# Kernel tuning notes

Hardware: AMD Instinct MI355X
Metric: run time of the kernel (lower is better)

The kernel has to match this reference:

```python
import jax, jax.numpy as jnp
import numpy as np

ALPHA = 2.0  # init alpha
B, N, E = 8, 100000, 3200000


def setup_inputs() -> dict:
    key = jax.random.key(0)
    k1, k2, k3, k4 = jax.random.split(key, 4)
    y = jax.random.normal(k1, (B, N), dtype=jnp.float32)
    t = jnp.zeros((1,), dtype=jnp.float32)  # unused by the math, kept for signature fidelity
    graph_edge_attr = jax.random.uniform(k2, (E,), dtype=jnp.float32)
    dist_w = jax.random.normal(k3, (E,), dtype=jnp.float32)  # distances.weight ([E,1] flattened)
    edge_index = jax.random.randint(k4, (2, E), 0, N, dtype=jnp.int64)
    return {"y": y, "t": t, "graph_edge_attr": graph_edge_attr, "dist_w": dist_w, "edge_index": edge_index}


def reference(y, t, graph_edge_attr, dist_w, edge_index):
    ei0 = edge_index[0]  # source node per edge [E]
    ei1 = edge_index[1]  # target node per edge [E]
    n = y.shape[1]
    # edge_attr = sigmoid(distances.weight) -> [E]
    edge_attr = jax.nn.sigmoid(dist_w)
    # deg = scatter_add(graph.edge_attr, edge_index[0], dim_size=N) -> [N]
    deg = jax.ops.segment_sum(graph_edge_attr, ei0, num_segments=n)
    deg_a = jnp.power(deg[ei0], ALPHA)  # [E], gathered per edge at source node
    # grad_m = sqrt(edge_attr) * -1 * min(y[:,ei1]/deg^a - y[:,ei0]/deg^a, 0) -> [B,E]
    diff = y[:, ei1] / deg_a - y[:, ei0] / deg_a
    grad_m = jnp.sqrt(edge_attr) * (-1.0) * jnp.minimum(diff, 0.0)
    # grad_norm = scatter_add(|grad_m|, ei0, dim=1, dim_size=N) -> [B,N]
    grad_norm = jnp.zeros_like(y).at[:, ei0].add(jnp.abs(grad_m))
    # run_pde is None -> return f (mask branch not taken)
    return 1.0 - grad_norm
```

## Files before the change

kernel.cpp:

```cpp
#include <hip/hip_runtime.h>
#include <hip/hip_fp16.h>

#define BATCH 8
#define S_LOG 9
#define SBUCKET 512
#define KC 256
#define CB 1024
#define TTILE 2048
#define EPT 8
#define SCAP 15360

static inline size_t alignup(size_t x) { return (x + 255) & ~(size_t)255; }

__device__ __forceinline__ unsigned bf16hi(unsigned u) {
    return (u + 0x7FFFu + ((u >> 16) & 1u)) >> 16;
}

__device__ __forceinline__ int aligned_chunk(int E) {
    return (((E + CB - 1) / CB) + 15) & ~15;
}


__global__ __launch_bounds__(256)
void count_transpose_kernel(const int* __restrict__ ei0, unsigned* __restrict__ counts,
                            const float* __restrict__ y, uint4* __restrict__ yT,
                            int E, int N, int Npad) {
    __shared__ unsigned cnt[KC];
    int tid = threadIdx.x;
    if (blockIdx.x >= CB) {
        int n = (blockIdx.x - CB) * 256 + tid;
        if (n < Npad) {
            uint4 o = make_uint4(0u, 0u, 0u, 0u);
            if (n < N) {
                unsigned p[8];
#pragma unroll
                for (int b = 0; b < BATCH; ++b)
                    p[b] = bf16hi(__float_as_uint(y[(size_t)b * N + n]));
                o = make_uint4(p[0] | (p[1] << 16), p[2] | (p[3] << 16),
                               p[4] | (p[5] << 16), p[6] | (p[7] << 16));
            }
            yT[n] = o;
        }
        return;
    }
    cnt[tid] = 0;
    __syncthreads();
    int chunk = aligned_chunk(E);
    int lo = blockIdx.x * chunk;
    int hi = min(lo + chunk, E);
    for (int bi = lo; bi < hi; bi += 1024) {
        int idx = bi + tid * 4;
        if (idx + 4 <= hi) {
            int4 v = *(const int4*)(ei0 + idx);
            atomicAdd(&cnt[(unsigned)v.x >> S_LOG], 1u);
            atomicAdd(&cnt[(unsigned)v.y >> S_LOG], 1u);
            atomicAdd(&cnt[(unsigned)v.z >> S_LOG], 1u);
            atomicAdd(&cnt[(unsigned)v.w >> S_LOG], 1u);
        } else {
#pragma unroll
            for (int j = 0; j < 4; ++j) {
                int i2 = idx + j;
                if (i2 < hi) atomicAdd(&cnt[(unsigned)ei0[i2] >> S_LOG], 1u);
            }
        }
    }
    __syncthreads();
    counts[(size_t)tid * CB + blockIdx.x] = cnt[tid];
}

__global__ __launch_bounds__(256)
void scanB1_kernel(const unsigned* __restrict__ counts, unsigned* __restrict__ base,
                   unsigned* __restrict__ tot) {
    __shared__ unsigned ssum[256];
    int k = blockIdx.x, tid = threadIdx.x;
    const uint4* row4 = (const uint4*)(counts + (size_t)k * CB);
    uint4 v = row4[tid];
    unsigned lsum = v.x + v.y + v.z + v.w;
    ssum[tid] = lsum;
    __syncthreads();
    for (int off = 1; off < 256; off <<= 1) {
        unsigned u = ssum[tid];
        unsigned a = (tid >= off) ? ssum[tid - off] : 0u;
        __syncthreads();
        ssum[tid] = u + a;
        __syncthreads();
    }
    unsigned ex = ssum[tid] - lsum;
    if (tid == 255) tot[k] = ssum[255];
    uint4 o;
    o.x = ex;
    o.y = ex + v.x;
    o.z = o.y + v.y;
    o.w = o.z + v.z;
    ((uint4*)(base + (size_t)k * CB))[tid] = o;
}

__global__ void scanC_kernel(const unsigned* __restrict__ tot,
                             unsigned* __restrict__ bb, int E, int K) {
    __shared__ unsigned sb[KC];
    int t = threadIdx.x;
    unsigned v = (t < K) ? tot[t] : 0u;
    sb[t] = v;
    __syncthreads();
    for (int off = 1; off < KC; off <<= 1) {
        unsigned u = sb[t];
        unsigned a = (t >= off) ? sb[t - off] : 0u;
        __syncthreads();
        sb[t] = u + a;
        __syncthreads();
    }
    bb[t] = sb[t] - v;
    if (t == KC - 1) bb[KC] = (unsigned)E;
}

__global__ __launch_bounds__(256)
void scatter_kernel(const int* __restrict__ ei0, const int* __restrict__ ei1,
                    const float* __restrict__ dw, const float* __restrict__ gea,
                    const unsigned* __restrict__ base, const unsigned* __restrict__ bb,
                    uint2* __restrict__ w0coef, int E) {
    __shared__ unsigned cursor[KC];
    __shared__ unsigned h[KC];
    __shared__ unsigned tstart[KC];
    __shared__ unsigned wsum[4];
    __shared__ uint2 srec[TTILE];
    __shared__ unsigned char skey[TTILE];
    int tid = threadIdx.x;
    cursor[tid] = base[(size_t)tid * CB + blockIdx.x] + bb[tid];
    int chunk = aligned_chunk(E);
    int lo = blockIdx.x * chunk;
    int hi = min(lo + chunk, E);
    __syncthreads();

    for (int tileLo = lo; tileLo < hi; tileLo += TTILE) {
        int tn = min(TTILE, hi - tileLo);
        h[tid] = 0;
        __syncthreads();

        int base_off = tid * EPT;
        unsigned k_r[EPT], w0_r[EPT], pk_r[EPT], rk_r[EPT];
        int s0a[EPT], s1a[EPT];
        float dwa[EPT], gea_a[EPT];
        bool anyv = base_off < tn;
        if (base_off + EPT <= tn) {
            const int4* p0 = (const int4*)(ei0 + tileLo + base_off);
            const int4* p1 = (const int4*)(ei1 + tileLo + base_off);
            const float4* pd = (const float4*)(dw + tileLo + base_off);
            const float4* pg = (const float4*)(gea + tileLo + base_off);
            int4 a0 = p0[0], a1 = p0[1];
            int4 b0 = p1[0], b1 = p1[1];
            float4 d0 = pd[0], d1 = pd[1];
            float4 g0 = pg[0], g1 = pg[1];
            s0a[0]=a0.x; s0a[1]=a0.y; s0a[2]=a0.z; s0a[3]=a0.w;
            s0a[4]=a1.x; s0a[5]=a1.y; s0a[6]=a1.z; s0a[7]=a1.w;
            s1a[0]=b0.x; s1a[1]=b0.y; s1a[2]=b0.z; s1a[3]=b0.w;
            s1a[4]=b1.x; s1a[5]=b1.y; s1a[6]=b1.z; s1a[7]=b1.w;
            dwa[0]=d0.x; dwa[1]=d0.y; dwa[2]=d0.z; dwa[3]=d0.w;
            dwa[4]=d1.x; dwa[5]=d1.y; dwa[6]=d1.z; dwa[7]=d1.w;
            gea_a[0]=g0.x; gea_a[1]=g0.y; gea_a[2]=g0.z; gea_a[3]=g0.w;
            gea_a[4]=g1.x; gea_a[5]=g1.y; gea_a[6]=g1.z; gea_a[7]=g1.w;
#pragma unroll
            for (int j = 0; j < EPT; ++j) k_r[j] = 0u;
#pragma unroll
            for (int j = 0; j < EPT; ++j) {
                unsigned k = (unsigned)s0a[j] >> S_LOG;
                unsigned s0l = (unsigned)(s0a[j] & (SBUCKET - 1));
                k_r[j] = k;
                w0_r[j] = (unsigned)s1a[j] | (s0l << 17);
                float sig = 1.0f / (1.0f + __expf(-dwa[j]));
                pk_r[j] = (bf16hi(__float_as_uint(sqrtf(sig))) << 16) |
                          bf16hi(__float_as_uint(gea_a[j]));
            }
#pragma unroll
            for (int j = 0; j < EPT; ++j)
                rk_r[j] = atomicAdd(&h[k_r[j]], 1u);
        } else {
#pragma unroll
            for (int j = 0; j < EPT; ++j) {
                int off = base_off + j;
                k_r[j] = 0xFFFFFFFFu;
                if (off < tn) {
                    int i = tileLo + off;
                    int s0v = ei0[i];
                    int s1v = ei1[i];
                    unsigned k = (unsigned)s0v >> S_LOG;
                    unsigned s0l = (unsigned)(s0v & (SBUCKET - 1));
                    k_r[j] = k;
                    w0_r[j] = (unsigned)s1v | (s0l << 17);
                    float sig = 1.0f / (1.0f + __expf(-dw[i]));
                    pk_r[j] = (bf16hi(__float_as_uint(sqrtf(sig))) << 16) |
                              bf16hi(__float_as_uint(gea[i]));
                }
            }
#pragma unroll
            for (int j = 0; j < EPT; ++j)
                if (k_r[j] != 0xFFFFFFFFu) rk_r[j] = atomicAdd(&h[k_r[j]], 1u);
        }
        bool fullv = base_off + EPT <= tn;
        __syncthreads();

        unsigned hv = h[tid];
        unsigned v = hv;
        unsigned lane = tid & 63;
        unsigned wv = tid >> 6;
#pragma unroll
        for (int off = 1; off < 64; off <<= 1) {
            unsigned t = __shfl_up(v, off, 64);
            if (lane >= off) v += t;
        }
        if (lane == 63) wsum[wv] = v;
        __syncthreads();
        unsigned addv = 0;
#pragma unroll
        for (unsigned w = 0; w < 4; ++w)
            if (w < wv) addv += wsum[w];
        tstart[tid] = v + addv - hv;
        __syncthreads();

        if (fullv) {
#pragma unroll
            for (int j = 0; j < EPT; ++j) {
                unsigned slot = tstart[k_r[j]] + rk_r[j];
                srec[slot] = make_uint2(w0_r[j], pk_r[j]);
                skey[slot] = (unsigned char)k_r[j];
            }
        } else if (anyv) {
#pragma unroll
            for (int j = 0; j < EPT; ++j)
                if (k_r[j] != 0xFFFFFFFFu) {
                    unsigned slot = tstart[k_r[j]] + rk_r[j];
                    srec[slot] = make_uint2(w0_r[j], pk_r[j]);
                    skey[slot] = (unsigned char)k_r[j];
                }
        }
        __syncthreads();

        for (int i = tid; i < tn; i += 256) {
            uint2 u = srec[i];
            unsigned k = skey[i];
            unsigned pos = cursor[k] + ((unsigned)i - tstart[k]);
            w0coef[pos] = u;
        }
        __syncthreads();
        cursor[tid] += h[tid];
        __syncthreads();
    }
}

__global__ __launch_bounds__(512)
void accum_kernel(const uint2* __restrict__ w0coef, const unsigned* __restrict__ bb,
                  const uint4* __restrict__ yT,
                  float* __restrict__ out, int N) {
    __shared__ uint2 srt[SCAP];
    __shared__ unsigned bcnt[SBUCKET];
    __shared__ unsigned boff[SBUCKET];
    __shared__ unsigned bcur[SBUCKET];
    __shared__ unsigned wsums[8];
    int k = blockIdx.x, tid = threadIdx.x;
    int n0 = k << S_LOG;
    unsigned lane = tid & 63;
    unsigned wvi = tid >> 6;

    unsigned lo = bb[k], hi = bb[k + 1];

    uint4 y0r = yT[n0 + tid];
    float y0f[8];
    {
        unsigned yw[4] = {y0r.x, y0r.y, y0r.z, y0r.w};
#pragma unroll
        for (int p = 0; p < 4; ++p) {
            y0f[2 * p]     = __uint_as_float(yw[p] << 16);
            y0f[2 * p + 1] = __uint_as_float(yw[p] & 0xFFFF0000u);
        }
    }
    float acc[8] = {0.f, 0.f, 0.f, 0.f, 0.f, 0.f, 0.f, 0.f};
    float dega = 0.f;

    for (unsigned cbase = lo; cbase < hi; cbase += SCAP) {
        unsigned cn = min((unsigned)SCAP, hi - cbase);
        bcnt[tid] = 0u;
        __syncthreads();
        for (unsigned i = tid; i < cn; i += 512)
            atomicAdd(&bcnt[w0coef[cbase + i].x >> 17], 1u);
        __syncthreads();
        unsigned myc = bcnt[tid];
        unsigned v = myc;
#pragma unroll
        for (int off = 1; off < 64; off <<= 1) {
            unsigned t = __shfl_up(v, off, 64);
            if (lane >= off) v += t;
        }
        if (lane == 63) wsums[wvi] = v;
        __syncthreads();
        unsigned add = 0;
#pragma unroll
        for (unsigned w = 0; w < 8; ++w)
            if (w < wvi) add += wsums[w];
        unsigned myoff = v + add - myc;
        boff[tid] = myoff;
        bcur[tid] = myoff;
        __syncthreads();
        for (unsigned i = tid; i < cn; i += 512) {
            uint2 r = w0coef[cbase + i];
            unsigned slot = atomicAdd(&bcur[r.x >> 17], 1u);
            srt[slot] = r;
        }
        __syncthreads();
        unsigned s = myoff, e = myoff + myc;
        uint2 r0 = make_uint2(0u, 0u), r1 = make_uint2(0u, 0u);
        uint4 g0 = make_uint4(0u, 0u, 0u, 0u), g1 = g0;
        if (s < e)     { r0 = srt[s];     g0 = yT[r0.x & 0x1FFFFu]; }
        if (s + 1 < e) { r1 = srt[s + 1]; g1 = yT[r1.x & 0x1FFFFu]; }
        for (unsigned i = s; i < e; ++i) {
            uint2 rc = r0; uint4 gc = g0;
            r0 = r1; g0 = g1;
            if (i + 2 < e) { r1 = srt[i + 2]; g1 = yT[r1.x & 0x1FFFFu]; }
            float cf = __uint_as_float(rc.y & 0xFFFF0000u);
            float ge = __uint_as_float(rc.y << 16);
            unsigned gw[4] = {gc.x, gc.y, gc.z, gc.w};
#pragma unroll
            for (int p = 0; p < 4; ++p) {
                float ga = __uint_as_float(gw[p] << 16);
                float gb = __uint_as_float(gw[p] & 0xFFFF0000u);
                acc[2 * p]     += cf * fmaxf(y0f[2 * p]     - ga, 0.0f);
                acc[2 * p + 1] += cf * fmaxf(y0f[2 * p + 1] - gb, 0.0f);
            }
            dega += ge;
        }
        __syncthreads();
    }

    int n = n0 + tid;
    if (n < N) {
        float invd = (dega != 0.0f) ? 1.0f / (dega * dega) : 0.0f;
#pragma unroll
        for (int b = 0; b < BATCH; ++b)
            out[(size_t)b * N + n] = 1.0f - acc[b] * invd;
    }
}


__global__ void fill_one_kernel(float* __restrict__ out, int n) {
    int i = blockIdx.x * blockDim.x + threadIdx.x;
    if (i < n) out[i] = 1.0f;
}

__global__ void zero_kernel(float* __restrict__ p, int n) {
    int i = blockIdx.x * blockDim.x + threadIdx.x;
    if (i < n) p[i] = 0.0f;
}

__global__ void deg_kernel(const float* __restrict__ gea,
                           const int* __restrict__ ei0,
                           float* __restrict__ deg, int E) {
    int e = blockIdx.x * blockDim.x + threadIdx.x;
    if (e < E) atomicAdd(&deg[ei0[e]], gea[e]);
}

__global__ void edge_kernel(const float* __restrict__ y,
                            const float* __restrict__ dw,
                            const int* __restrict__ ei0,
                            const int* __restrict__ ei1,
                            const float* __restrict__ deg,
                            float* __restrict__ out,
                            int E, int N) {
    int e = blockIdx.x * blockDim.x + threadIdx.x;
    if (e >= E) return;
    int s0 = ei0[e];
    int s1 = ei1[e];
    float d = deg[s0];
    float inv = 1.0f / (d * d);
    float sig = 1.0f / (1.0f + __expf(-dw[e]));
    float coef = sqrtf(sig) * inv;
#pragma unroll
    for (int b = 0; b < BATCH; ++b) {
        float y0 = y[(size_t)b * N + s0];
        float y1 = y[(size_t)b * N + s1];
        float gm = coef * fmaxf(y0 - y1, 0.0f);
        if (gm != 0.0f) atomicAdd(&out[(size_t)b * N + s0], -gm);
    }
}


extern "C" void kernel_launch(void* const* d_in, const int* in_sizes, int n_in,
                              void* d_out, int out_size, void* d_ws, size_t ws_size,
                              hipStream_t stream) {
    const float* y   = (const float*)d_in[0];
    const float* gea = (const float*)d_in[2];
    const float* dw  = (const float*)d_in[3];
    const int*   ei  = (const int*)d_in[4];

    const int E = in_sizes[2];
    const int N = in_sizes[0] / BATCH;
    const int* ei0 = ei;
    const int* ei1 = ei + E;

    const int K = (N + SBUCKET - 1) >> S_LOG;
    const int Npad = K << S_LOG;

    size_t o_yT     = 0;
    size_t o_rcf    = o_yT     + alignup((size_t)Npad * 16);
    size_t o_counts = o_rcf    + alignup((size_t)E * 8);
    size_t o_base   = o_counts + alignup((size_t)KC * CB * 4);
    size_t o_tot    = o_base   + alignup((size_t)KC * CB * 4);
    size_t o_bb     = o_tot    + alignup((size_t)KC * 4);
    size_t need     = o_bb     + alignup((size_t)(KC + 1) * 4);

    if (K <= KC && N <= 131071 && ws_size >= need) {
        char* w = (char*)d_ws;
        uint4*    yT     = (uint4*)(w + o_yT);
        uint2*    w0coef = (uint2*)(w + o_rcf);
        unsigned* counts = (unsigned*)(w + o_counts);
        unsigned* base   = (unsigned*)(w + o_base);
        unsigned* tot    = (unsigned*)(w + o_tot);
        unsigned* bb     = (unsigned*)(w + o_bb);

        int tb = (Npad + 255) / 256;
        count_transpose_kernel<<<CB + tb, 256, 0, stream>>>(ei0, counts, y, yT,
                                                            E, N, Npad);
        scanB1_kernel<<<K, 256, 0, stream>>>(counts, base, tot);
        scanC_kernel<<<1, KC, 0, stream>>>(tot, bb, E, K);
        scatter_kernel<<<CB, 256, 0, stream>>>(ei0, ei1, dw, gea, base, bb,
                                               w0coef, E);
        accum_kernel<<<K, 512, 0, stream>>>(w0coef, bb, yT, (float*)d_out, N);
    } else {
        float* deg = (float*)d_ws;
        zero_kernel<<<(N + 255) / 256, 256, 0, stream>>>(deg, N);
        fill_one_kernel<<<(out_size + 255) / 256, 256, 0, stream>>>((float*)d_out, out_size);
        deg_kernel<<<(E + 255) / 256, 256, 0, stream>>>(gea, ei0, deg, E);
        edge_kernel<<<(E + 255) / 256, 256, 0, stream>>>(y, dw, ei0, ei1, deg,
                                                         (float*)d_out, E, N);
    }
}
```

Measured before the change: 154.2 us.

## Replace bucketed two-level sort with per-node CSR counting sort via global atomics

Drops the coarse 512-node bucket histogram, the tiled shared-memory scatter and the per-block local sort in the accumulator. It now builds a full per-node CSR: global atomic degree counts, a two-level scan over nodes, and a scatter that places each edge directly with a global atomic cursor. The accumulator becomes one thread per node walking its contiguous edge range, with no shared-memory staging. This removes several shared-memory passes and barriers, but adds about 6.4M global atomics and uncoalesced 8-byte scattered writes, and each thread's edge-list length now depends on node degree, so work per thread is uneven.

After: 503.2 us. 3.26x slower.

```diff
diff --git a/kernel.cpp b/kernel.cpp
--- a/kernel.cpp
+++ b/kernel.cpp
@@ -6,9 +6,7 @@
 #define SBUCKET 512
 #define KC 256
 #define CB 1024
-#define TTILE 2048
 #define EPT 8
-#define SCAP 15360
 
 static inline size_t alignup(size_t x) { return (x + 255) & ~(size_t)255; }
 
@@ -22,10 +20,15 @@
 
 
 __global__ __launch_bounds__(256)
-void count_transpose_kernel(const int* __restrict__ ei0, unsigned* __restrict__ counts,
+void zero_deg_kernel(unsigned* __restrict__ deg, int Npad) {
+    int i = blockIdx.x * 256 + threadIdx.x;
+    if (i < Npad) deg[i] = 0u;
+}
+
+__global__ __launch_bounds__(256)
+void count_transpose_kernel(const int* __restrict__ ei0, unsigned* __restrict__ deg,
                             const float* __restrict__ y, uint4* __restrict__ yT,
                             int E, int N, int Npad) {
-    __shared__ unsigned cnt[KC];
     int tid = threadIdx.x;
     if (blockIdx.x >= CB) {
         int n = (blockIdx.x - CB) * 256 + tid;
@@ -43,8 +46,6 @@
         }
         return;
     }
-    cnt[tid] = 0;
-    __syncthreads();
     int chunk = aligned_chunk(E);
     int lo = blockIdx.x * chunk;
     int hi = min(lo + chunk, E);
@@ -52,51 +53,47 @@
         int idx = bi + tid * 4;
         if (idx + 4 <= hi) {
             int4 v = *(const int4*)(ei0 + idx);
-            atomicAdd(&cnt[(unsigned)v.x >> S_LOG], 1u);
-            atomicAdd(&cnt[(unsigned)v.y >> S_LOG], 1u);
-            atomicAdd(&cnt[(unsigned)v.z >> S_LOG], 1u);
-            atomicAdd(&cnt[(unsigned)v.w >> S_LOG], 1u);
+            atomicAdd(&deg[v.x], 1u);
+            atomicAdd(&deg[v.y], 1u);
+            atomicAdd(&deg[v.z], 1u);
+            atomicAdd(&deg[v.w], 1u);
         } else {
 #pragma unroll
             for (int j = 0; j < 4; ++j) {
                 int i2 = idx + j;
-                if (i2 < hi) atomicAdd(&cnt[(unsigned)ei0[i2] >> S_LOG], 1u);
+                if (i2 < hi) atomicAdd(&deg[ei0[i2]], 1u);
             }
         }
     }
+}
+
+__global__ __launch_bounds__(512)
+void scanN1_kernel(const unsigned* __restrict__ deg, unsigned* __restrict__ node_base,
+                   unsigned* __restrict__ tot) {
+    __shared__ unsigned wsums[8];
+    int k = blockIdx.x, tid = threadIdx.x;
+    unsigned lane = tid & 63;
+    unsigned wvi = tid >> 6;
+    int i = (k << S_LOG) + tid;
+    unsigned dv = deg[i];
+    unsigned v = dv;
+#pragma unroll
+    for (int off = 1; off < 64; off <<= 1) {
+        unsigned t = __shfl_up(v, off, 64);
+        if (lane >= off) v += t;
+    }
+    if (lane == 63) wsums[wvi] = v;
     __syncthreads();
-    counts[(size_t)tid * CB + blockIdx.x] = cnt[tid];
-}
-
-__global__ __launch_bounds__(256)
-void scanB1_kernel(const unsigned* __restrict__ counts, unsigned* __restrict__ base,
-                   unsigned* __restrict__ tot) {
-    __shared__ unsigned ssum[256];
-    int k = blockIdx.x, tid = threadIdx.x;
-    const uint4* row4 = (const uint4*)(counts + (size_t)k * CB);
-    uint4 v = row4[tid];
-    unsigned lsum = v.x + v.y + v.z + v.w;
-    ssum[tid] = lsum;
-    __syncthreads();
-    for (int off = 1; off < 256; off <<= 1) {
-        unsigned u = ssum[tid];
-        unsigned a = (tid >= off) ? ssum[tid - off] : 0u;
-        __syncthreads();
-        ssum[tid] = u + a;
-        __syncthreads();
-    }
-    unsigned ex = ssum[tid] - lsum;
-    if (tid == 255) tot[k] = ssum[255];
-    uint4 o;
-    o.x = ex;
-    o.y = ex + v.x;
-    o.z = o.y + v.y;
-    o.w = o.z + v.z;
-    ((uint4*)(base + (size_t)k * CB))[tid] = o;
+    unsigned add = 0;
+#pragma unroll
+    for (unsigned w = 0; w < 8; ++w)
+        if (w < wvi) add += wsums[w];
+    node_base[i] = v + add - dv;
+    if (tid == 511) tot[k] = v + add;
 }
 
 __global__ void scanC_kernel(const unsigned* __restrict__ tot,
-                             unsigned* __restrict__ bb, int E, int K) {
+                             unsigned* __restrict__ bb, int K) {
     __shared__ unsigned sb[KC];
     int t = threadIdx.x;
     unsigned v = (t < K) ? tot[t] : 0u;
@@ -110,46 +107,39 @@
         __syncthreads();
     }
     bb[t] = sb[t] - v;
-    if (t == KC - 1) bb[KC] = (unsigned)E;
+}
+
+__global__ __launch_bounds__(512)
+void scanN2_kernel(unsigned* __restrict__ node_base, unsigned* __restrict__ node_cur,
+                   const unsigned* __restrict__ bb) {
+    int k = blockIdx.x, tid = threadIdx.x;
+    int i = (k << S_LOG) + tid;
+    unsigned v = node_base[i] + bb[k];
+    node_base[i] = v;
+    node_cur[i] = v;
 }
 
 __global__ __launch_bounds__(256)
 void scatter_kernel(const int* __restrict__ ei0, const int* __restrict__ ei1,
                     const float* __restrict__ dw, const float* __restrict__ gea,
-                    const unsigned* __restrict__ base, const unsigned* __restrict__ bb,
-                    uint2* __restrict__ w0coef, int E) {
-    __shared__ unsigned cursor[KC];
-    __shared__ unsigned h[KC];
-    __shared__ unsigned tstart[KC];
-    __shared__ unsigned wsum[4];
-    __shared__ uint2 srec[TTILE];
-    __shared__ unsigned char skey[TTILE];
+                    unsigned* __restrict__ node_cur, uint2* __restrict__ w0coef, int E) {
     int tid = threadIdx.x;
-    cursor[tid] = base[(size_t)tid * CB + blockIdx.x] + bb[tid];
     int chunk = aligned_chunk(E);
     int lo = blockIdx.x * chunk;
     int hi = min(lo + chunk, E);
-    __syncthreads();
-
-    for (int tileLo = lo; tileLo < hi; tileLo += TTILE) {
-        int tn = min(TTILE, hi - tileLo);
-        h[tid] = 0;
-        __syncthreads();
-
-        int base_off = tid * EPT;
-        unsigned k_r[EPT], w0_r[EPT], pk_r[EPT], rk_r[EPT];
-        int s0a[EPT], s1a[EPT];
-        float dwa[EPT], gea_a[EPT];
-        bool anyv = base_off < tn;
-        if (base_off + EPT <= tn) {
-            const int4* p0 = (const int4*)(ei0 + tileLo + base_off);
-            const int4* p1 = (const int4*)(ei1 + tileLo + base_off);
-            const float4* pd = (const float4*)(dw + tileLo + base_off);
-            const float4* pg = (const float4*)(gea + tileLo + base_off);
+
+    for (int base_i = lo + tid * EPT; base_i < hi; base_i += 256 * EPT) {
+        if (base_i + EPT <= hi) {
+            const int4* p0 = (const int4*)(ei0 + base_i);
+            const int4* p1 = (const int4*)(ei1 + base_i);
+            const float4* pd = (const float4*)(dw + base_i);
+            const float4* pg = (const float4*)(gea + base_i);
             int4 a0 = p0[0], a1 = p0[1];
             int4 b0 = p1[0], b1 = p1[1];
             float4 d0 = pd[0], d1 = pd[1];
             float4 g0 = pg[0], g1 = pg[1];
+            int s0a[EPT], s1a[EPT];
+            float dwa[EPT], gea_a[EPT];
             s0a[0]=a0.x; s0a[1]=a0.y; s0a[2]=a0.z; s0a[3]=a0.w;
             s0a[4]=a1.x; s0a[5]=a1.y; s0a[6]=a1.z; s0a[7]=a1.w;
             s1a[0]=b0.x; s1a[1]=b0.y; s1a[2]=b0.z; s1a[3]=b0.w;
@@ -158,111 +148,41 @@
             dwa[4]=d1.x; dwa[5]=d1.y; dwa[6]=d1.z; dwa[7]=d1.w;
             gea_a[0]=g0.x; gea_a[1]=g0.y; gea_a[2]=g0.z; gea_a[3]=g0.w;
             gea_a[4]=g1.x; gea_a[5]=g1.y; gea_a[6]=g1.z; gea_a[7]=g1.w;
-#pragma unroll
-            for (int j = 0; j < EPT; ++j) k_r[j] = 0u;
+            unsigned pk[EPT], pos[EPT];
 #pragma unroll
             for (int j = 0; j < EPT; ++j) {
-                unsigned k = (unsigned)s0a[j] >> S_LOG;
-                unsigned s0l = (unsigned)(s0a[j] & (SBUCKET - 1));
-                k_r[j] = k;
-                w0_r[j] = (unsigned)s1a[j] | (s0l << 17);
                 float sig = 1.0f / (1.0f + __expf(-dwa[j]));
-                pk_r[j] = (bf16hi(__float_as_uint(sqrtf(sig))) << 16) |
-                          bf16hi(__float_as_uint(gea_a[j]));
+                pk[j] = (bf16hi(__float_as_uint(sqrtf(sig))) << 16) |
+                        bf16hi(__float_as_uint(gea_a[j]));
             }
 #pragma unroll
             for (int j = 0; j < EPT; ++j)
-                rk_r[j] = atomicAdd(&h[k_r[j]], 1u);
+                pos[j] = atomicAdd(&node_cur[s0a[j]], 1u);
+#pragma unroll
+            for (int j = 0; j < EPT; ++j)
+                w0coef[pos[j]] = make_uint2((unsigned)s1a[j], pk[j]);
         } else {
 #pragma unroll
             for (int j = 0; j < EPT; ++j) {
-                int off = base_off + j;
-                k_r[j] = 0xFFFFFFFFu;
-                if (off < tn) {
-                    int i = tileLo + off;
-                    int s0v = ei0[i];
-                    int s1v = ei1[i];
-                    unsigned k = (unsigned)s0v >> S_LOG;
-                    unsigned s0l = (unsigned)(s0v & (SBUCKET - 1));
-                    k_r[j] = k;
-                    w0_r[j] = (unsigned)s1v | (s0l << 17);
+                int i = base_i + j;
+                if (i < hi) {
                     float sig = 1.0f / (1.0f + __expf(-dw[i]));
-                    pk_r[j] = (bf16hi(__float_as_uint(sqrtf(sig))) << 16) |
-                              bf16hi(__float_as_uint(gea[i]));
+                    unsigned pk = (bf16hi(__float_as_uint(sqrtf(sig))) << 16) |
+                                  bf16hi(__float_as_uint(gea[i]));
+                    unsigned pos = atomicAdd(&node_cur[ei0[i]], 1u);
+                    w0coef[pos] = make_uint2((unsigned)ei1[i], pk);
                 }
             }
-#pragma unroll
-            for (int j = 0; j < EPT; ++j)
-                if (k_r[j] != 0xFFFFFFFFu) rk_r[j] = atomicAdd(&h[k_r[j]], 1u);
-        }
-        bool fullv = base_off + EPT <= tn;
-        __syncthreads();
-
-        unsigned hv = h[tid];
-        unsigned v = hv;
-        unsigned lane = tid & 63;
-        unsigned wv = tid >> 6;
-#pragma unroll
-        for (int off = 1; off < 64; off <<= 1) {
-            unsigned t = __shfl_up(v, off, 64);
-            if (lane >= off) v += t;
-        }
-        if (lane == 63) wsum[wv] = v;
-        __syncthreads();
-        unsigned addv = 0;
-#pragma unroll
-        for (unsigned w = 0; w < 4; ++w)
-            if (w < wv) addv += wsum[w];
-        tstart[tid] = v + addv - hv;
-        __syncthreads();
-
-        if (fullv) {
-#pragma unroll
-            for (int j = 0; j < EPT; ++j) {
-                unsigned slot = tstart[k_r[j]] + rk_r[j];
-                srec[slot] = make_uint2(w0_r[j], pk_r[j]);
-                skey[slot] = (unsigned char)k_r[j];
-            }
-        } else if (anyv) {
-#pragma unroll
-            for (int j = 0; j < EPT; ++j)
-                if (k_r[j] != 0xFFFFFFFFu) {
-                    unsigned slot = tstart[k_r[j]] + rk_r[j];
-                    srec[slot] = make_uint2(w0_r[j], pk_r[j]);
-                    skey[slot] = (unsigned char)k_r[j];
-                }
-        }
-        __syncthreads();
-
-        for (int i = tid; i < tn; i += 256) {
-            uint2 u = srec[i];
-            unsigned k = skey[i];
-            unsigned pos = cursor[k] + ((unsigned)i - tstart[k]);
-            w0coef[pos] = u;
-        }
-        __syncthreads();
-        cursor[tid] += h[tid];
-        __syncthreads();
-    }
-}
-
-__global__ __launch_bounds__(512)
-void accum_kernel(const uint2* __restrict__ w0coef, const unsigned* __restrict__ bb,
-                  const uint4* __restrict__ yT,
+        }
+    }
+}
+
+__global__ __launch_bounds__(256)
+void accum_kernel(const uint2* __restrict__ w0coef, const unsigned* __restrict__ node_base,
+                  const unsigned* __restrict__ deg, const uint4* __restrict__ yT,
                   float* __restrict__ out, int N) {
-    __shared__ uint2 srt[SCAP];
-    __shared__ unsigned bcnt[SBUCKET];
-    __shared__ unsigned boff[SBUCKET];
-    __shared__ unsigned bcur[SBUCKET];
-    __shared__ unsigned wsums[8];
-    int k = blockIdx.x, tid = threadIdx.x;
-    int n0 = k << S_LOG;
-    unsigned lane = tid & 63;
-    unsigned wvi = tid >> 6;
-
-    unsigned lo = bb[k], hi = bb[k + 1];
-
-    uint4 y0r = yT[n0 + tid];
+    int n = blockIdx.x * 256 + threadIdx.x;
+    uint4 y0r = yT[n];
     float y0f[8];
     {
         unsigned yw[4] = {y0r.x, y0r.y, y0r.z, y0r.w};
@@ -275,61 +195,31 @@
     float acc[8] = {0.f, 0.f, 0.f, 0.f, 0.f, 0.f, 0.f, 0.f};
     float dega = 0.f;
 
-    for (unsigned cbase = lo; cbase < hi; cbase += SCAP) {
-        unsigned cn = min((unsigned)SCAP, hi - cbase);
-        bcnt[tid] = 0u;
-        __syncthreads();
-        for (unsigned i = tid; i < cn; i += 512)
-            atomicAdd(&bcnt[w0coef[cbase + i].x >> 17], 1u);
-        __syncthreads();
-        unsigned myc = bcnt[tid];
-        unsigned v = myc;
-#pragma unroll
-        for (int off = 1; off < 64; off <<= 1) {
-            unsigned t = __shfl_up(v, off, 64);
-            if (lane >= off) v += t;
-        }
-        if (lane == 63) wsums[wvi] = v;
-        __syncthreads();
-        unsigned add = 0;
-#pragma unroll
-        for (unsigned w = 0; w < 8; ++w)
-            if (w < wvi) add += wsums[w];
-        unsigned myoff = v + add - myc;
-        boff[tid] = myoff;
-        bcur[tid] = myoff;
-        __syncthreads();
-        for (unsigned i = tid; i < cn; i += 512) {
-            uint2 r = w0coef[cbase + i];
-            unsigned slot = atomicAdd(&bcur[r.x >> 17], 1u);
-            srt[slot] = r;
-        }
-        __syncthreads();
-        unsigned s = myoff, e = myoff + myc;
-        uint2 r0 = make_uint2(0u, 0u), r1 = make_uint2(0u, 0u);
-        uint4 g0 = make_uint4(0u, 0u, 0u, 0u), g1 = g0;
-        if (s < e)     { r0 = srt[s];     g0 = yT[r0.x & 0x1FFFFu]; }
-        if (s + 1 < e) { r1 = srt[s + 1]; g1 = yT[r1.x & 0x1FFFFu]; }
-        for (unsigned i = s; i < e; ++i) {
-            uint2 rc = r0; uint4 gc = g0;
-            r0 = r1; g0 = g1;
-            if (i + 2 < e) { r1 = srt[i + 2]; g1 = yT[r1.x & 0x1FFFFu]; }
-            float cf = __uint_as_float(rc.y & 0xFFFF0000u);
-            float ge = __uint_as_float(rc.y << 16);
-            unsigned gw[4] = {gc.x, gc.y, gc.z, gc.w};
-#pragma unroll
-            for (int p = 0; p < 4; ++p) {
-                float ga = __uint_as_float(gw[p] << 16);
-                float gb = __uint_as_float(gw[p] & 0xFFFF0000u);
-                acc[2 * p]     += cf * fmaxf(y0f[2 * p]     - ga, 0.0f);
-                acc[2 * p + 1] += cf * fmaxf(y0f[2 * p + 1] - gb, 0.0f);
-            }
-            dega += ge;
-        }
-        __syncthreads();
-    }
-
-    int n = n0 + tid;
+    unsigned lo = node_base[n];
+    unsigned hi = lo + deg[n];
+    uint2 z2 = make_uint2(0u, 0u);
+    uint4 z4 = make_uint4(0u, 0u, 0u, 0u);
+    uint2 r0 = z2, r1 = z2;
+    uint4 g0 = z4, g1 = z4;
+    if (lo < hi)     { r0 = w0coef[lo];     g0 = yT[r0.x]; }
+    if (lo + 1 < hi) { r1 = w0coef[lo + 1]; g1 = yT[r1.x]; }
+    for (unsigned i = lo; i < hi; ++i) {
+        uint2 rc = r0; uint4 gc = g0;
+        r0 = r1; g0 = g1;
+        if (i + 2 < hi) { r1 = w0coef[i + 2]; g1 = yT[r1.x]; }
+        float cf = __uint_as_float(rc.y & 0xFFFF0000u);
+        float ge = __uint_as_float(rc.y << 16);
+        unsigned gw[4] = {gc.x, gc.y, gc.z, gc.w};
+#pragma unroll
+        for (int p = 0; p < 4; ++p) {
+            float ga = __uint_as_float(gw[p] << 16);
+            float gb = __uint_as_float(gw[p] & 0xFFFF0000u);
+            acc[2 * p]     += cf * fmaxf(y0f[2 * p]     - ga, 0.0f);
+            acc[2 * p + 1] += cf * fmaxf(y0f[2 * p + 1] - gb, 0.0f);
+        }
+        dega += ge;
+    }
+
     if (n < N) {
         float invd = (dega != 0.0f) ? 1.0f / (dega * dega) : 0.0f;
 #pragma unroll
@@ -399,29 +289,34 @@
 
     size_t o_yT     = 0;
     size_t o_rcf    = o_yT     + alignup((size_t)Npad * 16);
-    size_t o_counts = o_rcf    + alignup((size_t)E * 8);
-    size_t o_base   = o_counts + alignup((size_t)KC * CB * 4);
-    size_t o_tot    = o_base   + alignup((size_t)KC * CB * 4);
+    size_t o_deg    = o_rcf    + alignup((size_t)E * 8);
+    size_t o_nbase  = o_deg    + alignup((size_t)Npad * 4);
+    size_t o_ncur   = o_nbase  + alignup((size_t)Npad * 4);
+    size_t o_tot    = o_ncur   + alignup((size_t)Npad * 4);
     size_t o_bb     = o_tot    + alignup((size_t)KC * 4);
-    size_t need     = o_bb     + alignup((size_t)(KC + 1) * 4);
+    size_t need     = o_bb     + alignup((size_t)KC * 4);
 
     if (K <= KC && N <= 131071 && ws_size >= need) {
         char* w = (char*)d_ws;
         uint4*    yT     = (uint4*)(w + o_yT);
         uint2*    w0coef = (uint2*)(w + o_rcf);
-        unsigned* counts = (unsigned*)(w + o_counts);
-        unsigned* base   = (unsigned*)(w + o_base);
+        unsigned* deg    = (unsigned*)(w + o_deg);
+        unsigned* nbase  = (unsigned*)(w + o_nbase);
+        unsigned* ncur   = (unsigned*)(w + o_ncur);
         unsigned* tot    = (unsigned*)(w + o_tot);
         unsigned* bb     = (unsigned*)(w + o_bb);
 
         int tb = (Npad + 255) / 256;
-        count_transpose_kernel<<<CB + tb, 256, 0, stream>>>(ei0, counts, y, yT,
+        zero_deg_kernel<<<tb, 256, 0, stream>>>(deg, Npad);
+        count_transpose_kernel<<<CB + tb, 256, 0, stream>>>(ei0, deg, y, yT,
                                                             E, N, Npad);
-        scanB1_kernel<<<K, 256, 0, stream>>>(counts, base, tot);
-        scanC_kernel<<<1, KC, 0, stream>>>(tot, bb, E, K);
-        scatter_kernel<<<CB, 256, 0, stream>>>(ei0, ei1, dw, gea, base, bb,
+        scanN1_kernel<<<K, 512, 0, stream>>>(deg, nbase, tot);
+        scanC_kernel<<<1, KC, 0, stream>>>(tot, bb, K);
+        scanN2_kernel<<<K, 512, 0, stream>>>(nbase, ncur, bb);
+        scatter_kernel<<<CB, 256, 0, stream>>>(ei0, ei1, dw, gea, ncur,
                                                w0coef, E);
-        accum_kernel<<<K, 512, 0, stream>>>(w0coef, bb, yT, (float*)d_out, N);
+        accum_kernel<<<tb, 256, 0, stream>>>(w0coef, nbase, deg, yT,
+                                             (float*)d_out, N);
     } else {
         float* deg = (float*)d_ws;
         zero_kernel<<<(N + 255) / 256, 256, 0, stream>>>(deg, N);
```
